# Performance work log

Measured on AMD Instinct MI355X. Metric: run time of the kernel, lower is better.

## Reference

```python
import jax, jax.numpy as jnp
import numpy as np

H = 128
T = 120
F_IN = 180
BN_EPS = 1e-5
LEAKY_SLOPE = 0.01


def _lstm_layer(x, wih, whh, bih, bhh):
    """Single LSTM layer. x: (B,T,D); wih:(4H,D), whh:(4H,H). PyTorch gate order i,f,g,o."""
    B = x.shape[0]
    # Precompute input projections for all timesteps: (B,T,4H)
    x_proj = jnp.einsum('btd,gd->btg', x, wih) + bih + bhh
    x_proj = jnp.transpose(x_proj, (1, 0, 2))  # (T,B,4H) for scan over time
    h0 = jnp.zeros((B, H), dtype=x.dtype)
    c0 = jnp.zeros((B, H), dtype=x.dtype)

    def step(carry, xt):
        h, c = carry
        gates = xt + h @ whh.T  # (B,4H)
        i, f, g, o = jnp.split(gates, 4, axis=-1)
        i = jax.nn.sigmoid(i)
        f = jax.nn.sigmoid(f)
        g = jnp.tanh(g)
        o = jax.nn.sigmoid(o)
        c = f * c + i * g
        h = o * jnp.tanh(c)
        return (h, c), h

    (_, _), hs = jax.lax.scan(step, (h0, c0), x_proj)  # hs: (T,B,H)
    return jnp.transpose(hs, (1, 0, 2))  # (B,T,H)


def setup_inputs() -> dict:
    key = jax.random.key(0)
    ks = jax.random.split(key, 16)
    B = 2048
    s = 0.1  # keep activations in a stable range
    inp = {
        'x': jax.random.normal(ks[0], (B, F_IN, T), jnp.float32),
        'fc_w': jax.random.normal(ks[1], (H, F_IN), jnp.float32) * s,
        'fc_b': jax.random.normal(ks[2], (H,), jnp.float32) * s,
        'bn_g': jax.random.uniform(ks[3], (H,), jnp.float32, 0.5, 1.5),
        'bn_b': jax.random.normal(ks[4], (H,), jnp.float32) * s,
        'bn_mean': jax.random.normal(ks[5], (H,), jnp.float32) * s,
        'bn_var': jax.random.uniform(ks[6], (H,), jnp.float32, 0.5, 1.5),
        'wih0': jax.random.normal(ks[7], (4 * H, H), jnp.float32) * s,
        'whh0': jax.random.normal(ks[8], (4 * H, H), jnp.float32) * s,
        'bih0': jax.random.normal(ks[9], (4 * H,), jnp.float32) * s,
        'bhh0': jax.random.normal(ks[10], (4 * H,), jnp.float32) * s,
        'wih1': jax.random.normal(ks[11], (4 * H, H), jnp.float32) * s,
        'whh1': jax.random.normal(ks[12], (4 * H, H), jnp.float32) * s,
        'bih1': jax.random.normal(ks[13], (4 * H,), jnp.float32) * s,
        'bhh1': jax.random.normal(ks[14], (4 * H,), jnp.float32) * s,
    }
    return inp


def reference(x, fc_w, fc_b, bn_g, bn_b, bn_mean, bn_var,
              wih0, whh0, bih0, bhh0, wih1, whh1, bih1, bhh1):
    # x.reshape(-1,180,120).permute(0,2,1) -> (B,120,180)
    h = jnp.transpose(x.reshape(-1, F_IN, T), (0, 2, 1)).reshape(-1, F_IN)
    # Linear + BatchNorm1d (eval mode) + LeakyReLU
    h = h @ fc_w.T + fc_b
    h = (h - bn_mean) * jax.lax.rsqrt(bn_var + BN_EPS) * bn_g + bn_b
    h = jnp.where(h >= 0, h, LEAKY_SLOPE * h)
    h = h.reshape(-1, T, H)
    # 2-layer LSTM, take last timestep
    h = _lstm_layer(h, wih0, whh0, bih0, bhh0)
    h = _lstm_layer(h, wih1, whh1, bih1, bhh1)
    return h[:, -1, :]
```

## Files before the change

### kernel.cpp

```cpp
#include <hip/hip_runtime.h>

#define T_STEPS 120
#define NF_IN   180
#define H_DIM   128
#define G_DIM   512
#define K_FC    192
#define HP      136
#define XPR     12

typedef __attribute__((ext_vector_type(8))) short short8;
typedef __attribute__((ext_vector_type(4))) float f32x4;

#define LDS_BARRIER() asm volatile("s_waitcnt lgkmcnt(0)\ns_barrier" ::: "memory")

__device__ __forceinline__ f32x4 mfma16(short8 a, short8 b, f32x4 c) {
    return __builtin_amdgcn_mfma_f32_16x16x32_bf16(a, b, c, 0, 0, 0);
}

__device__ __forceinline__ short f2bf(float x) {
    union { float f; unsigned u; } v; v.f = x;
    unsigned r = v.u + 0x7fffu + ((v.u >> 16) & 1u);
    return (short)(r >> 16);
}

__device__ __forceinline__ float sig_y(float y) {
    return __builtin_amdgcn_rcpf(1.f + __expf(y));
}
__device__ __forceinline__ float tanh_y(float y) {
    return 1.f - 2.f * __builtin_amdgcn_rcpf(1.f + __expf(y));
}

__global__ void prep_kernel(
    const float* __restrict__ fc_w, const float* __restrict__ fc_b,
    const float* __restrict__ bn_g, const float* __restrict__ bn_b,
    const float* __restrict__ bn_mean, const float* __restrict__ bn_var,
    const float* __restrict__ wih0, const float* __restrict__ whh0,
    const float* __restrict__ bih0, const float* __restrict__ bhh0,
    const float* __restrict__ wih1, const float* __restrict__ whh1,
    const float* __restrict__ bih1, const float* __restrict__ bhh1,
    short* __restrict__ fcw_o, float* __restrict__ fcb_o,
    float* __restrict__ bias0_o, float* __restrict__ bias1_o,
    short* __restrict__ wih0_o, short* __restrict__ whh0_o,
    short* __restrict__ wih1_o, short* __restrict__ whh1_o)
{
    int tid = blockIdx.x * blockDim.x + threadIdx.x;
    int stride = gridDim.x * blockDim.x;
    for (int i = tid; i < H_DIM * K_FC; i += stride) {
        int h = i / K_FC, f = i % K_FC;
        float s = bn_g[h] * rsqrtf(bn_var[h] + 1e-5f);
        float v = (f < NF_IN) ? fc_w[h * NF_IN + f] * s : 0.f;
        fcw_o[i] = f2bf(v);
    }
    for (int i = tid; i < H_DIM; i += stride) {
        float s = bn_g[i] * rsqrtf(bn_var[i] + 1e-5f);
        fcb_o[i] = (fc_b[i] - bn_mean[i]) * s + bn_b[i];
    }
    for (int i = tid; i < G_DIM; i += stride) {
        float sc = ((i >> 7) == 2) ? 2.f : -1.f;
        bias0_o[i] = (bih0[i] + bhh0[i]) * sc;
        bias1_o[i] = (bih1[i] + bhh1[i]) * sc;
    }
    for (int i = tid; i < G_DIM * H_DIM; i += stride) {
        float sc = ((i >> 7) / H_DIM == 2) ? 2.f : -1.f;
        wih0_o[i] = f2bf(wih0[i] * sc); whh0_o[i] = f2bf(whh0[i] * sc);
        wih1_o[i] = f2bf(wih1[i] * sc); whh1_o[i] = f2bf(whh1[i] * sc);
    }
}

__global__ __launch_bounds__(256) void fc_kernel(
    const float* __restrict__ x, const short* __restrict__ fcw,
    const float* __restrict__ fcb, short* __restrict__ xfc)
{
    __shared__ short outs[120 * 132];
    const int b = blockIdx.x;
    const int tid = threadIdx.x;
    const int wave = tid >> 6, lane = tid & 63;
    const int m16 = lane & 15, q = lane >> 4;

    short8 af[2][6];
#pragma unroll
    for (int mi = 0; mi < 2; ++mi) {
        int t = (wave * 2 + mi) * 16 + m16;
        if (t > 119) t = 119;
        const float* xb = x + (size_t)b * (NF_IN * T_STEPS) + (size_t)q * 8 * T_STEPS + t;
#pragma unroll
        for (int kc = 0; kc < 6; ++kc) {
            union { short s[8]; short8 v; } u;
#pragma unroll
            for (int j = 0; j < 8; ++j) {
                int f = kc * 32 + q * 8 + j;
                float val = (f < NF_IN) ? xb[(kc * 32 + j) * T_STEPS] : 0.f;
                u.s[j] = f2bf(val);
            }
            af[mi][kc] = u.v;
        }
    }

    float fcb_v[8];
#pragma unroll
    for (int nt = 0; nt < 8; ++nt) fcb_v[nt] = fcb[nt * 16 + m16];

    f32x4 acc[2][8];
#pragma unroll
    for (int mi = 0; mi < 2; ++mi)
#pragma unroll
        for (int nt = 0; nt < 8; ++nt) acc[mi][nt] = (f32x4){0.f, 0.f, 0.f, 0.f};

#pragma unroll
    for (int nt = 0; nt < 8; ++nt) {
        short8 bf[6];
#pragma unroll
        for (int kc = 0; kc < 6; ++kc)
            bf[kc] = *(const short8*)(fcw + (nt * 16 + m16) * K_FC + kc * 32 + q * 8);
#pragma unroll
        for (int mi = 0; mi < 2; ++mi)
#pragma unroll
            for (int kc = 0; kc < 6; ++kc)
                acc[mi][nt] = mfma16(af[mi][kc], bf[kc], acc[mi][nt]);
    }

#pragma unroll
    for (int mi = 0; mi < 2; ++mi)
#pragma unroll
        for (int nt = 0; nt < 8; ++nt)
#pragma unroll
            for (int r = 0; r < 4; ++r) {
                int t = (wave * 2 + mi) * 16 + q * 4 + r;
                int h = nt * 16 + m16;
                float v = acc[mi][nt][r] + fcb_v[nt];
                v = (v >= 0.f) ? v : 0.01f * v;
                if (t < 120) outs[t * 132 + h] = f2bf(v);
            }
    __syncthreads();

    unsigned* dst = (unsigned*)xfc + (size_t)b * (T_STEPS * H_DIM / 2);
    const unsigned* srcs = (const unsigned*)outs;
    for (int i = tid; i < T_STEPS * H_DIM / 2; i += 256) {
        int t = i >> 6, c2 = i & 63;
        dst[i] = srcs[t * 66 + c2];
    }
}

__global__ __launch_bounds__(512, 2) void lstm_kernel(
    const short* h_in, const short* __restrict__ wih,
    const short* __restrict__ whh, const float* __restrict__ bias,
    short* h_out, float* __restrict__ fout)
{
    __shared__ short h_lds[2 * 8 * HP];
    __shared__ float xp_lds[2 * G_DIM * XPR];
    __shared__ float rc_lds[G_DIM * XPR];

    const int tid = threadIdx.x;
    const int w = tid >> 6, lane = tid & 63;
    const int m16 = lane & 15, q = lane >> 4, m8 = m16 & 7;
    const int b0 = blockIdx.x * 8;

    for (int i = tid; i < 8 * HP; i += 512) ((unsigned*)h_lds)[i] = 0u;

    short8 whf[4][4], wif[4][4];
    float bias_v[4];
#pragma unroll
    for (int g = 0; g < 4; ++g) {
        int n = g * 128 + w * 16 + m16;
        bias_v[g] = bias[n];
#pragma unroll
        for (int kc = 0; kc < 4; ++kc) {
            whf[g][kc] = *(const short8*)(whh + n * H_DIM + kc * 32 + q * 8);
            wif[g][kc] = *(const short8*)(wih + n * H_DIM + kc * 32 + q * 8);
        }
    }

    float c0 = 0.f, c1 = 0.f;

    auto loadPair = [&](short8 ax[4], int t1) {
        int t = t1 + (m16 >> 3);
        if (t > T_STEPS - 1) t = T_STEPS - 1;
        const short* src = h_in + ((size_t)(b0 + m8) * T_STEPS + t) * H_DIM + q * 8;
#pragma unroll
        for (int kc = 0; kc < 4; ++kc) ax[kc] = *(const short8*)(src + kc * 32);
    };

    auto recStep = [&](int rb) {
        const short* hb = h_lds + rb * (8 * HP) + m8 * HP + q * 8;
        short8 ar[4];
#pragma unroll
        for (int kc = 0; kc < 4; ++kc) ar[kc] = *(const short8*)(hb + kc * 32);
#pragma unroll
        for (int g = 0; g < 4; ++g) {
            f32x4 acc = (f32x4){0.f, 0.f, 0.f, 0.f};
#pragma unroll
            for (int kc = 0; kc < 4; ++kc) acc = mfma16(ar[kc], whf[g][kc], acc);
            if (q < 2)
                *(f32x4*)(rc_lds + (g * 128 + w * 16 + m16) * XPR + q * 4) = acc;
        }
    };

    auto update = [&](int s, int xb, int hb) {
        const float* xpb = xp_lds + xb * (G_DIM * XPR);
        float2 rd[4], xd[4];
#pragma unroll
        for (int g = 0; g < 4; ++g) {
            int n = (g * 128 + w * 16 + m16) * XPR + q * 2;
            rd[g] = *(const float2*)(rc_lds + n);
            xd[g] = *(const float2*)(xpb + n);
        }
        float i0 = sig_y(rd[0].x + xd[0].x), i1 = sig_y(rd[0].y + xd[0].y);
        float f0 = sig_y(rd[1].x + xd[1].x), f1 = sig_y(rd[1].y + xd[1].y);
        float g0 = tanh_y(rd[2].x + xd[2].x), g1 = tanh_y(rd[2].y + xd[2].y);
        float o0 = sig_y(rd[3].x + xd[3].x), o1 = sig_y(rd[3].y + xd[3].y);
        c0 = f0 * c0 + i0 * g0;
        c1 = f1 * c1 + i1 * g1;
        float h0v = o0 * tanh_y(2.f * c0);
        float h1v = o1 * tanh_y(2.f * c1);
        short* hw = h_lds + hb * (8 * HP);
        int dim = w * 16 + m16;
        hw[(q * 2) * HP + dim]     = f2bf(h0v);
        hw[(q * 2 + 1) * HP + dim] = f2bf(h1v);
        if (fout != nullptr && s == T_STEPS - 1) {
            fout[(size_t)(b0 + q * 2) * H_DIM + dim]     = h0v;
            fout[(size_t)(b0 + q * 2 + 1) * H_DIM + dim] = h1v;
        }
    };

    auto projPair = [&](short8 ax[4], int t1) {
        float* xpb = xp_lds + ((t1 + (q >> 1)) & 1) * (G_DIM * XPR);
#pragma unroll
        for (int g = 0; g < 4; ++g) {
            float bv = bias_v[g];
            f32x4 acc = (f32x4){bv, bv, bv, bv};
#pragma unroll
            for (int kc = 0; kc < 4; ++kc) acc = mfma16(ax[kc], wif[g][kc], acc);
            *(f32x4*)(xpb + (g * 128 + w * 16 + m16) * XPR + (q & 1) * 4) = acc;
        }
    };

    auto exportH = [&](int s, int hb) {
        int row = tid >> 6, c2 = tid & 63;
        unsigned v = ((const unsigned*)h_lds)[hb * (4 * HP) + row * (HP / 2) + c2];
        ((unsigned*)h_out)[((size_t)(b0 + row) * T_STEPS + s) * (H_DIM / 2) + c2] = v;
    };

    {
        short8 a0[4];
        const short* src = h_in + (size_t)(b0 + m8) * T_STEPS * H_DIM + q * 8;
#pragma unroll
        for (int kc = 0; kc < 4; ++kc) a0[kc] = *(const short8*)(src + kc * 32);
#pragma unroll
        for (int g = 0; g < 4; ++g) {
            float bv = bias_v[g];
            f32x4 acc = (f32x4){bv, bv, bv, bv};
#pragma unroll
            for (int kc = 0; kc < 4; ++kc) acc = mfma16(a0[kc], wif[g][kc], acc);
            if (q < 2)
                *(f32x4*)(xp_lds + (g * 128 + w * 16 + m16) * XPR + q * 4) = acc;
        }
    }
    short8 axc[4];
    loadPair(axc, 1);
    LDS_BARRIER();

    for (int it = 0; it < T_STEPS / 2; ++it) {
        const int s = 2 * it;
        short8 axn[4];
        loadPair(axn, s + 3);
        recStep(1);
        update(s, 0, 0);
        projPair(axc, s + 1);
        if (h_out != nullptr && s >= 1) exportH(s - 1, 1);
        LDS_BARRIER();
        recStep(0);
        update(s + 1, 1, 1);
#pragma unroll
        for (int kc = 0; kc < 4; ++kc) axc[kc] = axn[kc];
        if (h_out != nullptr) exportH(s, 0);
        LDS_BARRIER();
    }
    if (h_out != nullptr) exportH(T_STEPS - 1, 1);
}

static constexpr size_t OFF_FCW  = 0;
static constexpr size_t OFF_FCB  = 49152;
static constexpr size_t OFF_B0   = 49664;
static constexpr size_t OFF_B1   = 51712;
static constexpr size_t OFF_WIH0 = 53760;
static constexpr size_t OFF_WHH0 = 184832;
static constexpr size_t OFF_WIH1 = 315904;
static constexpr size_t OFF_WHH1 = 446976;
static constexpr size_t OFF_BUFA = 578048;

extern "C" void kernel_launch(void* const* d_in, const int* in_sizes, int n_in,
                              void* d_out, int out_size, void* d_ws, size_t ws_size,
                              hipStream_t stream) {
    const float* x       = (const float*)d_in[0];
    const float* fc_w    = (const float*)d_in[1];
    const float* fc_b    = (const float*)d_in[2];
    const float* bn_g    = (const float*)d_in[3];
    const float* bn_b    = (const float*)d_in[4];
    const float* bn_mean = (const float*)d_in[5];
    const float* bn_var  = (const float*)d_in[6];
    const float* wih0    = (const float*)d_in[7];
    const float* whh0    = (const float*)d_in[8];
    const float* bih0    = (const float*)d_in[9];
    const float* bhh0    = (const float*)d_in[10];
    const float* wih1    = (const float*)d_in[11];
    const float* whh1    = (const float*)d_in[12];
    const float* bih1    = (const float*)d_in[13];
    const float* bhh1    = (const float*)d_in[14];

    const int B = in_sizes[0] / (NF_IN * T_STEPS);

    char* ws = (char*)d_ws;
    short* fcw   = (short*)(ws + OFF_FCW);
    float* fcb   = (float*)(ws + OFF_FCB);
    float* bias0 = (float*)(ws + OFF_B0);
    float* bias1 = (float*)(ws + OFF_B1);
    short* wih0b = (short*)(ws + OFF_WIH0);
    short* whh0b = (short*)(ws + OFF_WHH0);
    short* wih1b = (short*)(ws + OFF_WIH1);
    short* whh1b = (short*)(ws + OFF_WHH1);
    short* bufA  = (short*)(ws + OFF_BUFA);

    prep_kernel<<<256, 256, 0, stream>>>(
        fc_w, fc_b, bn_g, bn_b, bn_mean, bn_var,
        wih0, whh0, bih0, bhh0, wih1, whh1, bih1, bhh1,
        fcw, fcb, bias0, bias1, wih0b, whh0b, wih1b, whh1b);

    fc_kernel<<<B, 256, 0, stream>>>(x, fcw, fcb, bufA);

    lstm_kernel<<<B / 8, 512, 0, stream>>>(bufA, wih0b, whh0b, bias0, bufA, nullptr);
    lstm_kernel<<<B / 8, 512, 0, stream>>>(bufA, wih1b, whh1b, bias1, nullptr, (float*)d_out);
}
```

Before: 582.3 us.

## Keep LSTM gate accumulators in registers and fold log2e into weights

```diff
diff --git a/kernel.cpp b/kernel.cpp
--- a/kernel.cpp
+++ b/kernel.cpp
@@ -6,12 +6,20 @@
 #define G_DIM   512
 #define K_FC    192
 #define HP      136
-#define XPR     12
+
+#define L2E      1.4426950408889634f
+#define TWO_L2E  2.8853900817779268f
 
 typedef __attribute__((ext_vector_type(8))) short short8;
 typedef __attribute__((ext_vector_type(4))) float f32x4;
 
 #define LDS_BARRIER() asm volatile("s_waitcnt lgkmcnt(0)\ns_barrier" ::: "memory")
+
+#if __has_builtin(__builtin_amdgcn_exp2f)
+#define EXP2(x) __builtin_amdgcn_exp2f(x)
+#else
+#define EXP2(x) __expf((x) * 0.6931471805599453f)
+#endif
 
 __device__ __forceinline__ f32x4 mfma16(short8 a, short8 b, f32x4 c) {
     return __builtin_amdgcn_mfma_f32_16x16x32_bf16(a, b, c, 0, 0, 0);
@@ -23,11 +31,11 @@
     return (short)(r >> 16);
 }
 
-__device__ __forceinline__ float sig_y(float y) {
-    return __builtin_amdgcn_rcpf(1.f + __expf(y));
-}
-__device__ __forceinline__ float tanh_y(float y) {
-    return 1.f - 2.f * __builtin_amdgcn_rcpf(1.f + __expf(y));
+__device__ __forceinline__ float sig2(float y) {
+    return __builtin_amdgcn_rcpf(1.f + EXP2(y));
+}
+__device__ __forceinline__ float tanh2(float y) {
+    return 1.f - 2.f * __builtin_amdgcn_rcpf(1.f + EXP2(y));
 }
 
 __global__ void prep_kernel(
@@ -56,12 +64,12 @@
         fcb_o[i] = (fc_b[i] - bn_mean[i]) * s + bn_b[i];
     }
     for (int i = tid; i < G_DIM; i += stride) {
-        float sc = ((i >> 7) == 2) ? 2.f : -1.f;
+        float sc = ((i >> 7) == 2) ? TWO_L2E : -L2E;
         bias0_o[i] = (bih0[i] + bhh0[i]) * sc;
         bias1_o[i] = (bih1[i] + bhh1[i]) * sc;
     }
     for (int i = tid; i < G_DIM * H_DIM; i += stride) {
-        float sc = ((i >> 7) / H_DIM == 2) ? 2.f : -1.f;
+        float sc = ((i >> 7) / H_DIM == 2) ? TWO_L2E : -L2E;
         wih0_o[i] = f2bf(wih0[i] * sc); whh0_o[i] = f2bf(whh0[i] * sc);
         wih1_o[i] = f2bf(wih1[i] * sc); whh1_o[i] = f2bf(whh1[i] * sc);
     }
@@ -147,8 +155,6 @@
     short* h_out, float* __restrict__ fout)
 {
     __shared__ short h_lds[2 * 8 * HP];
-    __shared__ float xp_lds[2 * G_DIM * XPR];
-    __shared__ float rc_lds[G_DIM * XPR];
 
     const int tid = threadIdx.x;
     const int w = tid >> 6, lane = tid & 63;
@@ -170,7 +176,8 @@
         }
     }
 
-    float c0 = 0.f, c1 = 0.f;
+    float c[4] = {0.f, 0.f, 0.f, 0.f};
+    f32x4 P[4];
 
     auto loadPair = [&](short8 ax[4], int t1) {
         int t = t1 + (m16 >> 3);
@@ -180,57 +187,51 @@
         for (int kc = 0; kc < 4; ++kc) ax[kc] = *(const short8*)(src + kc * 32);
     };
 
-    auto recStep = [&](int rb) {
-        const short* hb = h_lds + rb * (8 * HP) + m8 * HP + q * 8;
-        short8 ar[4];
-#pragma unroll
-        for (int kc = 0; kc < 4; ++kc) ar[kc] = *(const short8*)(hb + kc * 32);
-#pragma unroll
-        for (int g = 0; g < 4; ++g) {
-            f32x4 acc = (f32x4){0.f, 0.f, 0.f, 0.f};
-#pragma unroll
-            for (int kc = 0; kc < 4; ++kc) acc = mfma16(ar[kc], whf[g][kc], acc);
-            if (q < 2)
-                *(f32x4*)(rc_lds + (g * 128 + w * 16 + m16) * XPR + q * 4) = acc;
-        }
-    };
-
-    auto update = [&](int s, int xb, int hb) {
-        const float* xpb = xp_lds + xb * (G_DIM * XPR);
-        float2 rd[4], xd[4];
-#pragma unroll
-        for (int g = 0; g < 4; ++g) {
-            int n = (g * 128 + w * 16 + m16) * XPR + q * 2;
-            rd[g] = *(const float2*)(rc_lds + n);
-            xd[g] = *(const float2*)(xpb + n);
-        }
-        float i0 = sig_y(rd[0].x + xd[0].x), i1 = sig_y(rd[0].y + xd[0].y);
-        float f0 = sig_y(rd[1].x + xd[1].x), f1 = sig_y(rd[1].y + xd[1].y);
-        float g0 = tanh_y(rd[2].x + xd[2].x), g1 = tanh_y(rd[2].y + xd[2].y);
-        float o0 = sig_y(rd[3].x + xd[3].x), o1 = sig_y(rd[3].y + xd[3].y);
-        c0 = f0 * c0 + i0 * g0;
-        c1 = f1 * c1 + i1 * g1;
-        float h0v = o0 * tanh_y(2.f * c0);
-        float h1v = o1 * tanh_y(2.f * c1);
-        short* hw = h_lds + hb * (8 * HP);
-        int dim = w * 16 + m16;
-        hw[(q * 2) * HP + dim]     = f2bf(h0v);
-        hw[(q * 2 + 1) * HP + dim] = f2bf(h1v);
-        if (fout != nullptr && s == T_STEPS - 1) {
-            fout[(size_t)(b0 + q * 2) * H_DIM + dim]     = h0v;
-            fout[(size_t)(b0 + q * 2 + 1) * H_DIM + dim] = h1v;
-        }
-    };
-
-    auto projPair = [&](short8 ax[4], int t1) {
-        float* xpb = xp_lds + ((t1 + (q >> 1)) & 1) * (G_DIM * XPR);
+    auto projPairR = [&](const short8 ax[4]) {
 #pragma unroll
         for (int g = 0; g < 4; ++g) {
             float bv = bias_v[g];
             f32x4 acc = (f32x4){bv, bv, bv, bv};
 #pragma unroll
             for (int kc = 0; kc < 4; ++kc) acc = mfma16(ax[kc], wif[g][kc], acc);
-            *(f32x4*)(xpb + (g * 128 + w * 16 + m16) * XPR + (q & 1) * 4) = acc;
+            P[g] = acc;
+        }
+    };
+
+    auto recUpdate = [&](int s, int rb, int hb, const f32x4 xp0, const f32x4 xp1,
+                         const f32x4 xp2, const f32x4 xp3) {
+        const short* rbp = h_lds + rb * (8 * HP) + m8 * HP + q * 8;
+        short8 ar[4];
+#pragma unroll
+        for (int kc = 0; kc < 4; ++kc) ar[kc] = *(const short8*)(rbp + kc * 32);
+        f32x4 a0 = xp0, a1 = xp1, a2 = xp2, a3 = xp3;
+#pragma unroll
+        for (int kc = 0; kc < 4; ++kc) {
+            a0 = mfma16(ar[kc], whf[0][kc], a0);
+            a1 = mfma16(ar[kc], whf[1][kc], a1);
+            a2 = mfma16(ar[kc], whf[2][kc], a2);
+            a3 = mfma16(ar[kc], whf[3][kc], a3);
+        }
+        float hv[4];
+#pragma unroll
+        for (int r = 0; r < 4; ++r) {
+            float i_ = sig2(a0[r]);
+            float f_ = sig2(a1[r]);
+            float g_ = tanh2(a2[r]);
+            float o_ = sig2(a3[r]);
+            c[r] = f_ * c[r] + i_ * g_;
+            hv[r] = o_ * tanh2(c[r] * TWO_L2E);
+        }
+        const int dim = w * 16 + m16;
+        if (q < 2) {
+            short* hw = h_lds + hb * (8 * HP) + (q * 4) * HP + dim;
+#pragma unroll
+            for (int r = 0; r < 4; ++r) hw[r * HP] = f2bf(hv[r]);
+        }
+        if (fout != nullptr && s == T_STEPS - 1 && q < 2) {
+#pragma unroll
+            for (int r = 0; r < 4; ++r)
+                fout[(size_t)(b0 + q * 4 + r) * H_DIM + dim] = hv[r];
         }
     };
 
@@ -241,19 +242,11 @@
     };
 
     {
-        short8 a0[4];
+        short8 ax0[4];
         const short* src = h_in + (size_t)(b0 + m8) * T_STEPS * H_DIM + q * 8;
 #pragma unroll
-        for (int kc = 0; kc < 4; ++kc) a0[kc] = *(const short8*)(src + kc * 32);
-#pragma unroll
-        for (int g = 0; g < 4; ++g) {
-            float bv = bias_v[g];
-            f32x4 acc = (f32x4){bv, bv, bv, bv};
-#pragma unroll
-            for (int kc = 0; kc < 4; ++kc) acc = mfma16(a0[kc], wif[g][kc], acc);
-            if (q < 2)
-                *(f32x4*)(xp_lds + (g * 128 + w * 16 + m16) * XPR + q * 4) = acc;
-        }
+        for (int kc = 0; kc < 4; ++kc) ax0[kc] = *(const short8*)(src + kc * 32);
+        projPairR(ax0);
     }
     short8 axc[4];
     loadPair(axc, 1);
@@ -263,13 +256,16 @@
         const int s = 2 * it;
         short8 axn[4];
         loadPair(axn, s + 3);
-        recStep(1);
-        update(s, 0, 0);
-        projPair(axc, s + 1);
+        f32x4 xps[4];
+#pragma unroll
+        for (int g = 0; g < 4; ++g)
+#pragma unroll
+            for (int e = 0; e < 4; ++e) xps[g][e] = __shfl_xor(P[g][e], 32);
+        recUpdate(s, 1, 0, xps[0], xps[1], xps[2], xps[3]);
+        projPairR(axc);
         if (h_out != nullptr && s >= 1) exportH(s - 1, 1);
         LDS_BARRIER();
-        recStep(0);
-        update(s + 1, 1, 1);
+        recUpdate(s + 1, 0, 1, P[0], P[1], P[2], P[3]);
 #pragma unroll
         for (int kc = 0; kc < 4; ++kc) axc[kc] = axn[kc];
         if (h_out != nullptr) exportH(s, 0);
```

Measured after the change: 585.9 us. No clear change (+0.6%).
